# Performance work log

Measured on AMD Instinct MI355X. Metric: run time of the kernel, lower is better.

## Reference

```python
import jax, jax.numpy as jnp
import numpy as np

N_NODES = 50000
N_EDGES = 500000
D_FEAT = 128


def setup_inputs() -> dict:
    key = jax.random.key(0)
    k1, k2, k3 = jax.random.split(key, 3)
    r = jax.random.normal(k1, (N_NODES, D_FEAT), dtype=jnp.float32)
    e = jax.random.normal(k2, (N_EDGES, D_FEAT), dtype=jnp.float32)
    a = jax.random.randint(k3, (N_EDGES, 2), 0, N_NODES, dtype=jnp.int64)
    return {"r": r, "e": e, "a": a}


def reference(r, e, a):
    # message: gather source/target node features along edges, scale by edge feats
    rij = r[a[:, 0]] * e  # [E, D] messages src -> dst
    rji = r[a[:, 1]] * e  # [E, D] messages dst -> src
    # aggregate: scatter_add into node dimension (fixed num_segments for jit)
    out = jax.ops.segment_sum(rij, a[:, 1], num_segments=r.shape[0])
    out = out + jax.ops.segment_sum(rji, a[:, 0], num_segments=r.shape[0])
    return out  # [N, D]
```

## Files before the change

kernel.cpp:

```cpp
#include <hip/hip_runtime.h>


#define D_FEAT 128
#define SCAN_TILE 1024

__device__ inline unsigned bf16pack2(float a, float b) {
    unsigned ua = __float_as_uint(a), ub = __float_as_uint(b);
    ua += 0x7fffu + ((ua >> 16) & 1u);
    ub += 0x7fffu + ((ub >> 16) & 1u);
    return ((ua >> 16) & 0xffffu) | (ub & 0xffff0000u);
}

__global__ void prep_kernel(const float* __restrict__ e,
                            const float* __restrict__ r,
                            const int* __restrict__ a,
                            uint2* __restrict__ e16,
                            uint2* __restrict__ r16,
                            int* __restrict__ deg,
                            int n_e4, int n_r4, int n_entries) {
    int gid = blockIdx.x * blockDim.x + threadIdx.x;
    if (gid < n_entries) atomicAdd(&deg[a[gid]], 1);
    if (gid < n_r4) {
        const float4 v = ((const float4*)r)[gid];
        uint2 p;
        p.x = bf16pack2(v.x, v.y);
        p.y = bf16pack2(v.z, v.w);
        r16[gid] = p;
    }
    if (gid >= n_e4) return;
    const float4 v = ((const float4*)e)[gid];
    uint2 p;
    p.x = bf16pack2(v.x, v.y);
    p.y = bf16pack2(v.z, v.w);
    e16[gid] = p;
}

__global__ void scanA_kernel(const int* __restrict__ deg, int* __restrict__ bsum,
                             int n) {
    __shared__ int wsum[16];
    int t = threadIdx.x, lane = t & 63, w = t >> 6;
    int i = blockIdx.x * SCAN_TILE + t;
    int v = (i < n) ? deg[i] : 0;
    #pragma unroll
    for (int off = 32; off > 0; off >>= 1) v += __shfl_down(v, off, 64);
    if (lane == 0) wsum[w] = v;
    __syncthreads();
    if (t == 0) {
        int s = 0;
        #pragma unroll
        for (int k = 0; k < 16; ++k) s += wsum[k];
        bsum[blockIdx.x] = s;
    }
}

__global__ void scanB_kernel(int* __restrict__ bsum, int* __restrict__ bbase,
                             int* __restrict__ offs, int nblk, int n) {
    if (threadIdx.x == 0) {
        int run = 0;
        for (int b = 0; b < nblk; ++b) {
            bbase[b] = run;
            run += bsum[b];
        }
        offs[n] = run;
    }
}

__global__ void scanC_kernel(int* __restrict__ deg, int* __restrict__ offs,
                             const int* __restrict__ bbase, int n) {
    __shared__ int wsum[16];
    int t = threadIdx.x, lane = t & 63, w = t >> 6;
    int i = blockIdx.x * SCAN_TILE + t;
    int v = (i < n) ? deg[i] : 0;
    int x = v;
    #pragma unroll
    for (int off = 1; off < 64; off <<= 1) {
        int y = __shfl_up(x, off, 64);
        if (lane >= off) x += y;
    }
    if (lane == 63) wsum[w] = x;
    __syncthreads();
    if (w == 0 && lane < 16) {
        int s = wsum[lane];
        #pragma unroll
        for (int off = 1; off < 16; off <<= 1) {
            int y = __shfl_up(s, off, 64);
            if (lane >= off) s += y;
        }
        wsum[lane] = s;
    }
    __syncthreads();
    int wbase = (w == 0) ? 0 : wsum[w - 1];
    if (i < n) {
        int excl = x - v + wbase + bbase[blockIdx.x];
        offs[i] = excl;
        deg[i] = excl;
    }
}

__global__ void fill_kernel(const int* __restrict__ a, int* __restrict__ cursor,
                            int2* __restrict__ pl, int n_entries) {
    int k = blockIdx.x * blockDim.x + threadIdx.x;
    if (k >= n_entries) return;
    int edge = k >> 1, j = k & 1;
    int other  = a[2 * edge + j];
    int center = a[2 * edge + (j ^ 1)];
    int pos = atomicAdd(&cursor[center], 1);
    pl[pos] = make_int2(edge, other);
}

__global__ __launch_bounds__(256) void gather_kernel(
    const unsigned* __restrict__ e16, const unsigned* __restrict__ r16,
    const int* __restrict__ offs, const int2* __restrict__ pl,
    float* __restrict__ out, int n_nodes) {
    int n = blockIdx.x * 4 + (threadIdx.x >> 6);
    if (n >= n_nodes) return;
    int lane = threadIdx.x & 63;
    int start = offs[n];
    int end = offs[n + 1];
    float accx = 0.f, accy = 0.f;
    int i = start;
    for (; i + 4 <= end; i += 4) {
        int2 p0 = pl[i];
        int2 p1 = pl[i + 1];
        int2 p2 = pl[i + 2];
        int2 p3 = pl[i + 3];
        unsigned ew0 = e16[(size_t)p0.x * 64 + lane];
        unsigned rw0 = r16[(size_t)p0.y * 64 + lane];
        unsigned ew1 = e16[(size_t)p1.x * 64 + lane];
        unsigned rw1 = r16[(size_t)p1.y * 64 + lane];
        unsigned ew2 = e16[(size_t)p2.x * 64 + lane];
        unsigned rw2 = r16[(size_t)p2.y * 64 + lane];
        unsigned ew3 = e16[(size_t)p3.x * 64 + lane];
        unsigned rw3 = r16[(size_t)p3.y * 64 + lane];
        accx += __uint_as_float(ew0 << 16) * __uint_as_float(rw0 << 16);
        accy += __uint_as_float(ew0 & 0xffff0000u) * __uint_as_float(rw0 & 0xffff0000u);
        accx += __uint_as_float(ew1 << 16) * __uint_as_float(rw1 << 16);
        accy += __uint_as_float(ew1 & 0xffff0000u) * __uint_as_float(rw1 & 0xffff0000u);
        accx += __uint_as_float(ew2 << 16) * __uint_as_float(rw2 << 16);
        accy += __uint_as_float(ew2 & 0xffff0000u) * __uint_as_float(rw2 & 0xffff0000u);
        accx += __uint_as_float(ew3 << 16) * __uint_as_float(rw3 << 16);
        accy += __uint_as_float(ew3 & 0xffff0000u) * __uint_as_float(rw3 & 0xffff0000u);
    }
    for (; i < end; ++i) {
        int2 p0 = pl[i];
        unsigned ew0 = e16[(size_t)p0.x * 64 + lane];
        unsigned rw0 = r16[(size_t)p0.y * 64 + lane];
        accx += __uint_as_float(ew0 << 16) * __uint_as_float(rw0 << 16);
        accy += __uint_as_float(ew0 & 0xffff0000u) * __uint_as_float(rw0 & 0xffff0000u);
    }
    float2 res;
    res.x = accx;
    res.y = accy;
    *((float2*)(out + (size_t)n * D_FEAT) + lane) = res;
}

__global__ void hist_kernel(const int* __restrict__ a, int* __restrict__ deg,
                            int n_elems) {
    int i = blockIdx.x * blockDim.x + threadIdx.x;
    if (i < n_elems) atomicAdd(&deg[a[i]], 1);
}

__global__ __launch_bounds__(256) void gather_f32_kernel(
    const float* __restrict__ r, const float* __restrict__ e,
    const int* __restrict__ offs, const int2* __restrict__ pl,
    float* __restrict__ out, int n_nodes) {
    int n = blockIdx.x * 4 + (threadIdx.x >> 6);
    if (n >= n_nodes) return;
    int lane = threadIdx.x & 63;
    int start = offs[n];
    int end = offs[n + 1];
    float accx = 0.f, accy = 0.f;
    for (int i = start; i < end; ++i) {
        int2 p0 = pl[i];
        float2 ev0 = *((const float2*)(e + (size_t)p0.x * D_FEAT) + lane);
        float2 rv0 = *((const float2*)(r + (size_t)p0.y * D_FEAT) + lane);
        accx += ev0.x * rv0.x;
        accy += ev0.y * rv0.y;
    }
    float2 res;
    res.x = accx;
    res.y = accy;
    *((float2*)(out + (size_t)n * D_FEAT) + lane) = res;
}

__global__ void mp_scatter_kernel(const float* __restrict__ r,
                                  const float* __restrict__ e,
                                  const int* __restrict__ a,
                                  float* __restrict__ out,
                                  int n_edges) {
    long long gid = (long long)blockIdx.x * blockDim.x + threadIdx.x;
    int edge = (int)(gid >> 7);
    int feat = (int)(gid & 127);
    if (edge >= n_edges) return;
    int s = a[2 * edge];
    int d = a[2 * edge + 1];
    float ev = e[(long long)edge * D_FEAT + feat];
    float rs = r[(long long)s * D_FEAT + feat];
    float rd = r[(long long)d * D_FEAT + feat];
    atomicAdd(&out[(long long)d * D_FEAT + feat], rs * ev);
    atomicAdd(&out[(long long)s * D_FEAT + feat], rd * ev);
}

extern "C" void kernel_launch(void* const* d_in, const int* in_sizes, int n_in,
                              void* d_out, int out_size, void* d_ws, size_t ws_size,
                              hipStream_t stream) {
    const float* r = (const float*)d_in[0];
    const float* e = (const float*)d_in[1];
    const int*   a = (const int*)d_in[2];
    float* out = (float*)d_out;

    int n_nodes   = in_sizes[0] / D_FEAT;
    int n_edges   = in_sizes[1] / D_FEAT;
    int n_entries = 2 * n_edges;
    int n_e4      = in_sizes[1] / 4;
    int n_r4      = in_sizes[0] / 4;

    int block = 256;
    int grid_e = (n_entries + block - 1) / block;
    int nblk_scan = (n_nodes + SCAN_TILE - 1) / SCAN_TILE;

    {
        size_t ints_head = (size_t)n_nodes + (size_t)(n_nodes + 1)
                         + 2 * (size_t)nblk_scan;
        ints_head = (ints_head + 1) & ~(size_t)1;
        size_t need = ((size_t)n_e4 + (size_t)n_r4) * sizeof(uint2)
                    + ints_head * sizeof(int)
                    + (size_t)n_entries * sizeof(int2);
        if (ws_size >= need && nblk_scan <= 1024) {
            uint2* e16  = (uint2*)d_ws;
            uint2* r16  = e16 + n_e4;
            int*   deg  = (int*)(r16 + n_r4);
            int*   offs = deg + n_nodes;
            int*   bsum = offs + n_nodes + 1;
            int*   bbase= bsum + nblk_scan;
            int2*  pl   = (int2*)((int*)(r16 + n_r4) + ints_head);

            hipMemsetAsync(deg, 0, (size_t)n_nodes * sizeof(int), stream);
            int grid_p = (n_e4 + block - 1) / block;
            prep_kernel<<<grid_p, block, 0, stream>>>(e, r, a, e16, r16, deg,
                                                      n_e4, n_r4, n_entries);
            scanA_kernel<<<nblk_scan, SCAN_TILE, 0, stream>>>(deg, bsum, n_nodes);
            scanB_kernel<<<1, 64, 0, stream>>>(bsum, bbase, offs, nblk_scan,
                                               n_nodes);
            scanC_kernel<<<nblk_scan, SCAN_TILE, 0, stream>>>(deg, offs, bbase,
                                                              n_nodes);
            fill_kernel<<<grid_e, block, 0, stream>>>(a, deg, pl, n_entries);
            int grid_g = (n_nodes + 3) / 4;
            gather_kernel<<<grid_g, 256, 0, stream>>>(
                (const unsigned*)e16, (const unsigned*)r16, offs, pl, out,
                n_nodes);
            return;
        }
    }

    {
        size_t ints_head = (size_t)n_nodes + (size_t)(n_nodes + 1)
                         + 2 * (size_t)nblk_scan;
        ints_head = (ints_head + 1) & ~(size_t)1;
        size_t need = ints_head * sizeof(int) + (size_t)n_entries * sizeof(int2);
        if (ws_size >= need && nblk_scan <= 1024) {
            int*  deg  = (int*)d_ws;
            int*  offs = deg + n_nodes;
            int*  bsum = offs + n_nodes + 1;
            int*  bbase= bsum + nblk_scan;
            int2* pl   = (int2*)((int*)d_ws + ints_head);

            hipMemsetAsync(deg, 0, (size_t)n_nodes * sizeof(int), stream);
            hist_kernel<<<grid_e, block, 0, stream>>>(a, deg, n_entries);
            scanA_kernel<<<nblk_scan, SCAN_TILE, 0, stream>>>(deg, bsum, n_nodes);
            scanB_kernel<<<1, 64, 0, stream>>>(bsum, bbase, offs, nblk_scan,
                                               n_nodes);
            scanC_kernel<<<nblk_scan, SCAN_TILE, 0, stream>>>(deg, offs, bbase,
                                                              n_nodes);
            fill_kernel<<<grid_e, block, 0, stream>>>(a, deg, pl, n_entries);
            int grid_g = (n_nodes + 3) / 4;
            gather_f32_kernel<<<grid_g, 256, 0, stream>>>(r, e, offs, pl, out,
                                                          n_nodes);
            return;
        }
    }

    hipMemsetAsync(d_out, 0, (size_t)out_size * sizeof(float), stream);
    long long total = (long long)n_edges * D_FEAT;
    long long grid = (total + block - 1) / block;
    mp_scatter_kernel<<<(int)grid, block, 0, stream>>>(r, e, a, out, n_edges);
}
```

Before: 550.2 us.

## Materialize per-edge fp16 messages in CSR order, then sum contiguously per node

Adds a path where each edge computes both of its messages from the fp32 inputs. It packs them to fp16 and writes them into slots taken from the per-node cursor, so the messages land grouped by destination node. A second kernel then reduces each node's contiguous message rows. This swaps the random gather of bf16 edge rows for a large scatter write plus a sequential read. It needs a workspace of about 256 MB and changes the reduced-precision format from bf16 to fp16.

New measurement: 596.3 us. 1.08x slower.

```diff
diff --git a/kernel.cpp b/kernel.cpp
--- a/kernel.cpp
+++ b/kernel.cpp
@@ -1,8 +1,20 @@
 #include <hip/hip_runtime.h>
+#include <hip/hip_fp16.h>
 
 
 #define D_FEAT 128
 #define SCAN_TILE 1024
+
+__device__ inline unsigned pack_h2(float a, float b) {
+    __half2 h;
+    h.x = __float2half_rn(a);
+    h.y = __float2half_rn(b);
+    return *reinterpret_cast<unsigned*>(&h);
+}
+__device__ inline float2 unpack_h2(unsigned u) {
+    __half2 h = *reinterpret_cast<__half2*>(&u);
+    return __half22float2(h);
+}
 
 __device__ inline unsigned bf16pack2(float a, float b) {
     unsigned ua = __float_as_uint(a), ub = __float_as_uint(b);
@@ -10,6 +22,131 @@
     ub += 0x7fffu + ((ub >> 16) & 1u);
     return ((ua >> 16) & 0xffffu) | (ub & 0xffff0000u);
 }
+
+__global__ void hist_kernel(const int* __restrict__ a, int* __restrict__ deg,
+                            int n_elems) {
+    int i = blockIdx.x * blockDim.x + threadIdx.x;
+    if (i < n_elems) atomicAdd(&deg[a[i]], 1);
+}
+
+__global__ void scanA_kernel(const int* __restrict__ deg, int* __restrict__ bsum,
+                             int n) {
+    __shared__ int wsum[16];
+    int t = threadIdx.x, lane = t & 63, w = t >> 6;
+    int i = blockIdx.x * SCAN_TILE + t;
+    int v = (i < n) ? deg[i] : 0;
+    #pragma unroll
+    for (int off = 32; off > 0; off >>= 1) v += __shfl_down(v, off, 64);
+    if (lane == 0) wsum[w] = v;
+    __syncthreads();
+    if (t == 0) {
+        int s = 0;
+        #pragma unroll
+        for (int k = 0; k < 16; ++k) s += wsum[k];
+        bsum[blockIdx.x] = s;
+    }
+}
+
+__global__ void scanB_kernel(int* __restrict__ bsum, int* __restrict__ bbase,
+                             int* __restrict__ offs, int nblk, int n) {
+    if (threadIdx.x == 0) {
+        int run = 0;
+        for (int b = 0; b < nblk; ++b) {
+            bbase[b] = run;
+            run += bsum[b];
+        }
+        offs[n] = run;
+    }
+}
+
+__global__ void scanC_kernel(int* __restrict__ deg, int* __restrict__ offs,
+                             const int* __restrict__ bbase, int n) {
+    __shared__ int wsum[16];
+    int t = threadIdx.x, lane = t & 63, w = t >> 6;
+    int i = blockIdx.x * SCAN_TILE + t;
+    int v = (i < n) ? deg[i] : 0;
+    int x = v;
+    #pragma unroll
+    for (int off = 1; off < 64; off <<= 1) {
+        int y = __shfl_up(x, off, 64);
+        if (lane >= off) x += y;
+    }
+    if (lane == 63) wsum[w] = x;
+    __syncthreads();
+    if (w == 0 && lane < 16) {
+        int s = wsum[lane];
+        #pragma unroll
+        for (int off = 1; off < 16; off <<= 1) {
+            int y = __shfl_up(s, off, 64);
+            if (lane >= off) s += y;
+        }
+        wsum[lane] = s;
+    }
+    __syncthreads();
+    int wbase = (w == 0) ? 0 : wsum[w - 1];
+    if (i < n) {
+        int excl = x - v + wbase + bbase[blockIdx.x];
+        offs[i] = excl;
+        deg[i] = excl;
+    }
+}
+
+__global__ __launch_bounds__(256) void msg_kernel(
+    const float* __restrict__ r, const float* __restrict__ e,
+    const int* __restrict__ a, int* __restrict__ cursor,
+    unsigned* __restrict__ msg, int n_edges) {
+    int k = blockIdx.x * 4 + (threadIdx.x >> 6);
+    if (k >= n_edges) return;
+    int lane = threadIdx.x & 63;
+    int s = a[2 * k];
+    int d = a[2 * k + 1];
+    int p0 = 0, p1 = 0;
+    if (lane == 0) {
+        p0 = atomicAdd(&cursor[d], 1);
+        p1 = atomicAdd(&cursor[s], 1);
+    }
+    float2 ev = *((const float2*)(e + (size_t)k * D_FEAT) + lane);
+    float2 rs = *((const float2*)(r + (size_t)s * D_FEAT) + lane);
+    float2 rd = *((const float2*)(r + (size_t)d * D_FEAT) + lane);
+    p0 = __shfl(p0, 0, 64);
+    p1 = __shfl(p1, 0, 64);
+    msg[(size_t)p0 * 64 + lane] = pack_h2(ev.x * rs.x, ev.y * rs.y);
+    msg[(size_t)p1 * 64 + lane] = pack_h2(ev.x * rd.x, ev.y * rd.y);
+}
+
+__global__ __launch_bounds__(256) void sum_kernel(
+    const unsigned* __restrict__ msg, const int* __restrict__ offs,
+    float* __restrict__ out, int n_nodes) {
+    int n = blockIdx.x * 4 + (threadIdx.x >> 6);
+    if (n >= n_nodes) return;
+    int lane = threadIdx.x & 63;
+    int start = offs[n];
+    int end = offs[n + 1];
+    float accx = 0.f, accy = 0.f;
+    int i = start;
+    for (; i + 4 <= end; i += 4) {
+        unsigned u0 = msg[(size_t)(i + 0) * 64 + lane];
+        unsigned u1 = msg[(size_t)(i + 1) * 64 + lane];
+        unsigned u2 = msg[(size_t)(i + 2) * 64 + lane];
+        unsigned u3 = msg[(size_t)(i + 3) * 64 + lane];
+        float2 f0 = unpack_h2(u0);
+        float2 f1 = unpack_h2(u1);
+        float2 f2 = unpack_h2(u2);
+        float2 f3 = unpack_h2(u3);
+        accx += f0.x + f1.x + f2.x + f3.x;
+        accy += f0.y + f1.y + f2.y + f3.y;
+    }
+    for (; i < end; ++i) {
+        float2 f0 = unpack_h2(msg[(size_t)i * 64 + lane]);
+        accx += f0.x;
+        accy += f0.y;
+    }
+    float2 res;
+    res.x = accx;
+    res.y = accy;
+    *((float2*)(out + (size_t)n * D_FEAT) + lane) = res;
+}
+
 
 __global__ void prep_kernel(const float* __restrict__ e,
                             const float* __restrict__ r,
@@ -33,68 +170,6 @@
     p.x = bf16pack2(v.x, v.y);
     p.y = bf16pack2(v.z, v.w);
     e16[gid] = p;
-}
-
-__global__ void scanA_kernel(const int* __restrict__ deg, int* __restrict__ bsum,
-                             int n) {
-    __shared__ int wsum[16];
-    int t = threadIdx.x, lane = t & 63, w = t >> 6;
-    int i = blockIdx.x * SCAN_TILE + t;
-    int v = (i < n) ? deg[i] : 0;
-    #pragma unroll
-    for (int off = 32; off > 0; off >>= 1) v += __shfl_down(v, off, 64);
-    if (lane == 0) wsum[w] = v;
-    __syncthreads();
-    if (t == 0) {
-        int s = 0;
-        #pragma unroll
-        for (int k = 0; k < 16; ++k) s += wsum[k];
-        bsum[blockIdx.x] = s;
-    }
-}
-
-__global__ void scanB_kernel(int* __restrict__ bsum, int* __restrict__ bbase,
-                             int* __restrict__ offs, int nblk, int n) {
-    if (threadIdx.x == 0) {
-        int run = 0;
-        for (int b = 0; b < nblk; ++b) {
-            bbase[b] = run;
-            run += bsum[b];
-        }
-        offs[n] = run;
-    }
-}
-
-__global__ void scanC_kernel(int* __restrict__ deg, int* __restrict__ offs,
-                             const int* __restrict__ bbase, int n) {
-    __shared__ int wsum[16];
-    int t = threadIdx.x, lane = t & 63, w = t >> 6;
-    int i = blockIdx.x * SCAN_TILE + t;
-    int v = (i < n) ? deg[i] : 0;
-    int x = v;
-    #pragma unroll
-    for (int off = 1; off < 64; off <<= 1) {
-        int y = __shfl_up(x, off, 64);
-        if (lane >= off) x += y;
-    }
-    if (lane == 63) wsum[w] = x;
-    __syncthreads();
-    if (w == 0 && lane < 16) {
-        int s = wsum[lane];
-        #pragma unroll
-        for (int off = 1; off < 16; off <<= 1) {
-            int y = __shfl_up(s, off, 64);
-            if (lane >= off) s += y;
-        }
-        wsum[lane] = s;
-    }
-    __syncthreads();
-    int wbase = (w == 0) ? 0 : wsum[w - 1];
-    if (i < n) {
-        int excl = x - v + wbase + bbase[blockIdx.x];
-        offs[i] = excl;
-        deg[i] = excl;
-    }
 }
 
 __global__ void fill_kernel(const int* __restrict__ a, int* __restrict__ cursor,
@@ -154,12 +229,6 @@
     *((float2*)(out + (size_t)n * D_FEAT) + lane) = res;
 }
 
-__global__ void hist_kernel(const int* __restrict__ a, int* __restrict__ deg,
-                            int n_elems) {
-    int i = blockIdx.x * blockDim.x + threadIdx.x;
-    if (i < n_elems) atomicAdd(&deg[a[i]], 1);
-}
-
 __global__ __launch_bounds__(256) void gather_f32_kernel(
     const float* __restrict__ r, const float* __restrict__ e,
     const int* __restrict__ offs, const int2* __restrict__ pl,
@@ -222,6 +291,34 @@
     {
         size_t ints_head = (size_t)n_nodes + (size_t)(n_nodes + 1)
                          + 2 * (size_t)nblk_scan;
+        ints_head = (ints_head + 63) & ~(size_t)63;
+        size_t need = ints_head * sizeof(int)
+                    + (size_t)n_entries * 64 * sizeof(unsigned);
+        if (ws_size >= need && nblk_scan <= 1024) {
+            int* deg   = (int*)d_ws;
+            int* offs  = deg + n_nodes;
+            int* bsum  = offs + n_nodes + 1;
+            int* bbase = bsum + nblk_scan;
+            unsigned* msg = (unsigned*)((int*)d_ws + ints_head);
+
+            hipMemsetAsync(deg, 0, (size_t)n_nodes * sizeof(int), stream);
+            hist_kernel<<<grid_e, block, 0, stream>>>(a, deg, n_entries);
+            scanA_kernel<<<nblk_scan, SCAN_TILE, 0, stream>>>(deg, bsum, n_nodes);
+            scanB_kernel<<<1, 64, 0, stream>>>(bsum, bbase, offs, nblk_scan,
+                                               n_nodes);
+            scanC_kernel<<<nblk_scan, SCAN_TILE, 0, stream>>>(deg, offs, bbase,
+                                                              n_nodes);
+            int grid_m = (n_edges + 3) / 4;
+            msg_kernel<<<grid_m, 256, 0, stream>>>(r, e, a, deg, msg, n_edges);
+            int grid_g = (n_nodes + 3) / 4;
+            sum_kernel<<<grid_g, 256, 0, stream>>>(msg, offs, out, n_nodes);
+            return;
+        }
+    }
+
+    {
+        size_t ints_head = (size_t)n_nodes + (size_t)(n_nodes + 1)
+                         + 2 * (size_t)nblk_scan;
         ints_head = (ints_head + 1) & ~(size_t)1;
         size_t need = ((size_t)n_e4 + (size_t)n_r4) * sizeof(uint2)
                     + ints_head * sizeof(int)
```

## Pad degree counters to cache-line stride and switch staging precision to fp16

Applied to the files above, without the earlier changes.

Spreads each node's degree/cursor counter across a 32-int (128-byte) stride so atomics from the histogram and fill kernels land on separate cache lines, aiming to reduce atomic contention. It also replaces bf16 packing with fp16 conversion for the staged edge and node features, which improves mantissa precision but risks overflow or underflow for large or tiny values. The counter memset and scan reads grow by the stride factor, so the scans now make strided, uncoalesced loads.

After: 561.5 us. +2.1%, slower.

```diff
diff --git a/kernel.cpp b/kernel.cpp
--- a/kernel.cpp
+++ b/kernel.cpp
@@ -1,14 +1,20 @@
 #include <hip/hip_runtime.h>
+#include <hip/hip_fp16.h>
 
 
 #define D_FEAT 128
 #define SCAN_TILE 1024
-
-__device__ inline unsigned bf16pack2(float a, float b) {
-    unsigned ua = __float_as_uint(a), ub = __float_as_uint(b);
-    ua += 0x7fffu + ((ua >> 16) & 1u);
-    ub += 0x7fffu + ((ub >> 16) & 1u);
-    return ((ua >> 16) & 0xffffu) | (ub & 0xffff0000u);
+#define CSTRIDE 32
+
+__device__ inline unsigned pack_h2(float a, float b) {
+    __half2 h;
+    h.x = __float2half_rn(a);
+    h.y = __float2half_rn(b);
+    return *reinterpret_cast<unsigned*>(&h);
+}
+__device__ inline float2 unpack_h2(unsigned u) {
+    __half2 h = *reinterpret_cast<__half2*>(&u);
+    return __half22float2(h);
 }
 
 __global__ void prep_kernel(const float* __restrict__ e,
@@ -16,31 +22,37 @@
                             const int* __restrict__ a,
                             uint2* __restrict__ e16,
                             uint2* __restrict__ r16,
-                            int* __restrict__ deg,
-                            int n_e4, int n_r4, int n_entries) {
+                            int* __restrict__ degp,
+                            int n_e4, int n_r4, int n_entries, int cstride) {
     int gid = blockIdx.x * blockDim.x + threadIdx.x;
-    if (gid < n_entries) atomicAdd(&deg[a[gid]], 1);
+    if (gid < n_entries) atomicAdd(&degp[(size_t)a[gid] * cstride], 1);
     if (gid < n_r4) {
         const float4 v = ((const float4*)r)[gid];
         uint2 p;
-        p.x = bf16pack2(v.x, v.y);
-        p.y = bf16pack2(v.z, v.w);
+        p.x = pack_h2(v.x, v.y);
+        p.y = pack_h2(v.z, v.w);
         r16[gid] = p;
     }
     if (gid >= n_e4) return;
     const float4 v = ((const float4*)e)[gid];
     uint2 p;
-    p.x = bf16pack2(v.x, v.y);
-    p.y = bf16pack2(v.z, v.w);
+    p.x = pack_h2(v.x, v.y);
+    p.y = pack_h2(v.z, v.w);
     e16[gid] = p;
 }
 
-__global__ void scanA_kernel(const int* __restrict__ deg, int* __restrict__ bsum,
-                             int n) {
+__global__ void hist_kernel(const int* __restrict__ a, int* __restrict__ degp,
+                            int n_elems, int cstride) {
+    int i = blockIdx.x * blockDim.x + threadIdx.x;
+    if (i < n_elems) atomicAdd(&degp[(size_t)a[i] * cstride], 1);
+}
+
+__global__ void scanA_kernel(const int* __restrict__ degp, int* __restrict__ bsum,
+                             int n, int cstride) {
     __shared__ int wsum[16];
     int t = threadIdx.x, lane = t & 63, w = t >> 6;
     int i = blockIdx.x * SCAN_TILE + t;
-    int v = (i < n) ? deg[i] : 0;
+    int v = (i < n) ? degp[(size_t)i * cstride] : 0;
     #pragma unroll
     for (int off = 32; off > 0; off >>= 1) v += __shfl_down(v, off, 64);
     if (lane == 0) wsum[w] = v;
@@ -65,12 +77,12 @@
     }
 }
 
-__global__ void scanC_kernel(int* __restrict__ deg, int* __restrict__ offs,
-                             const int* __restrict__ bbase, int n) {
+__global__ void scanC_kernel(int* __restrict__ degp, int* __restrict__ offs,
+                             const int* __restrict__ bbase, int n, int cstride) {
     __shared__ int wsum[16];
     int t = threadIdx.x, lane = t & 63, w = t >> 6;
     int i = blockIdx.x * SCAN_TILE + t;
-    int v = (i < n) ? deg[i] : 0;
+    int v = (i < n) ? degp[(size_t)i * cstride] : 0;
     int x = v;
     #pragma unroll
     for (int off = 1; off < 64; off <<= 1) {
@@ -93,18 +105,18 @@
     if (i < n) {
         int excl = x - v + wbase + bbase[blockIdx.x];
         offs[i] = excl;
-        deg[i] = excl;
-    }
-}
-
-__global__ void fill_kernel(const int* __restrict__ a, int* __restrict__ cursor,
-                            int2* __restrict__ pl, int n_entries) {
+        degp[(size_t)i * cstride] = excl;
+    }
+}
+
+__global__ void fill_kernel(const int* __restrict__ a, int* __restrict__ cursorp,
+                            int2* __restrict__ pl, int n_entries, int cstride) {
     int k = blockIdx.x * blockDim.x + threadIdx.x;
     if (k >= n_entries) return;
     int edge = k >> 1, j = k & 1;
     int other  = a[2 * edge + j];
     int center = a[2 * edge + (j ^ 1)];
-    int pos = atomicAdd(&cursor[center], 1);
+    int pos = atomicAdd(&cursorp[(size_t)center * cstride], 1);
     pl[pos] = make_int2(edge, other);
 }
 
@@ -132,32 +144,26 @@
         unsigned rw2 = r16[(size_t)p2.y * 64 + lane];
         unsigned ew3 = e16[(size_t)p3.x * 64 + lane];
         unsigned rw3 = r16[(size_t)p3.y * 64 + lane];
-        accx += __uint_as_float(ew0 << 16) * __uint_as_float(rw0 << 16);
-        accy += __uint_as_float(ew0 & 0xffff0000u) * __uint_as_float(rw0 & 0xffff0000u);
-        accx += __uint_as_float(ew1 << 16) * __uint_as_float(rw1 << 16);
-        accy += __uint_as_float(ew1 & 0xffff0000u) * __uint_as_float(rw1 & 0xffff0000u);
-        accx += __uint_as_float(ew2 << 16) * __uint_as_float(rw2 << 16);
-        accy += __uint_as_float(ew2 & 0xffff0000u) * __uint_as_float(rw2 & 0xffff0000u);
-        accx += __uint_as_float(ew3 << 16) * __uint_as_float(rw3 << 16);
-        accy += __uint_as_float(ew3 & 0xffff0000u) * __uint_as_float(rw3 & 0xffff0000u);
+        float2 e0 = unpack_h2(ew0), r0 = unpack_h2(rw0);
+        float2 e1 = unpack_h2(ew1), r1 = unpack_h2(rw1);
+        float2 e2 = unpack_h2(ew2), r2 = unpack_h2(rw2);
+        float2 e3 = unpack_h2(ew3), r3 = unpack_h2(rw3);
+        accx += e0.x * r0.x; accy += e0.y * r0.y;
+        accx += e1.x * r1.x; accy += e1.y * r1.y;
+        accx += e2.x * r2.x; accy += e2.y * r2.y;
+        accx += e3.x * r3.x; accy += e3.y * r3.y;
     }
     for (; i < end; ++i) {
         int2 p0 = pl[i];
         unsigned ew0 = e16[(size_t)p0.x * 64 + lane];
         unsigned rw0 = r16[(size_t)p0.y * 64 + lane];
-        accx += __uint_as_float(ew0 << 16) * __uint_as_float(rw0 << 16);
-        accy += __uint_as_float(ew0 & 0xffff0000u) * __uint_as_float(rw0 & 0xffff0000u);
+        float2 e0 = unpack_h2(ew0), r0 = unpack_h2(rw0);
+        accx += e0.x * r0.x; accy += e0.y * r0.y;
     }
     float2 res;
     res.x = accx;
     res.y = accy;
     *((float2*)(out + (size_t)n * D_FEAT) + lane) = res;
-}
-
-__global__ void hist_kernel(const int* __restrict__ a, int* __restrict__ deg,
-                            int n_elems) {
-    int i = blockIdx.x * blockDim.x + threadIdx.x;
-    if (i < n_elems) atomicAdd(&deg[a[i]], 1);
 }
 
 __global__ __launch_bounds__(256) void gather_f32_kernel(
@@ -220,7 +226,7 @@
     int nblk_scan = (n_nodes + SCAN_TILE - 1) / SCAN_TILE;
 
     {
-        size_t ints_head = (size_t)n_nodes + (size_t)(n_nodes + 1)
+        size_t ints_head = (size_t)CSTRIDE * n_nodes + (size_t)(n_nodes + 1)
                          + 2 * (size_t)nblk_scan;
         ints_head = (ints_head + 1) & ~(size_t)1;
         size_t need = ((size_t)n_e4 + (size_t)n_r4) * sizeof(uint2)
@@ -229,22 +235,26 @@
         if (ws_size >= need && nblk_scan <= 1024) {
             uint2* e16  = (uint2*)d_ws;
             uint2* r16  = e16 + n_e4;
-            int*   deg  = (int*)(r16 + n_r4);
-            int*   offs = deg + n_nodes;
+            int*   degp = (int*)(r16 + n_r4);
+            int*   offs = degp + (size_t)CSTRIDE * n_nodes;
             int*   bsum = offs + n_nodes + 1;
             int*   bbase= bsum + nblk_scan;
             int2*  pl   = (int2*)((int*)(r16 + n_r4) + ints_head);
 
-            hipMemsetAsync(deg, 0, (size_t)n_nodes * sizeof(int), stream);
+            hipMemsetAsync(degp, 0, (size_t)CSTRIDE * n_nodes * sizeof(int),
+                           stream);
             int grid_p = (n_e4 + block - 1) / block;
-            prep_kernel<<<grid_p, block, 0, stream>>>(e, r, a, e16, r16, deg,
-                                                      n_e4, n_r4, n_entries);
-            scanA_kernel<<<nblk_scan, SCAN_TILE, 0, stream>>>(deg, bsum, n_nodes);
+            prep_kernel<<<grid_p, block, 0, stream>>>(e, r, a, e16, r16, degp,
+                                                      n_e4, n_r4, n_entries,
+                                                      CSTRIDE);
+            scanA_kernel<<<nblk_scan, SCAN_TILE, 0, stream>>>(degp, bsum,
+                                                              n_nodes, CSTRIDE);
             scanB_kernel<<<1, 64, 0, stream>>>(bsum, bbase, offs, nblk_scan,
                                                n_nodes);
-            scanC_kernel<<<nblk_scan, SCAN_TILE, 0, stream>>>(deg, offs, bbase,
-                                                              n_nodes);
-            fill_kernel<<<grid_e, block, 0, stream>>>(a, deg, pl, n_entries);
+            scanC_kernel<<<nblk_scan, SCAN_TILE, 0, stream>>>(degp, offs, bbase,
+                                                              n_nodes, CSTRIDE);
+            fill_kernel<<<grid_e, block, 0, stream>>>(a, degp, pl, n_entries,
+                                                      CSTRIDE);
             int grid_g = (n_nodes + 3) / 4;
             gather_kernel<<<grid_g, 256, 0, stream>>>(
                 (const unsigned*)e16, (const unsigned*)r16, offs, pl, out,
@@ -254,29 +264,37 @@
     }
 
     {
-        size_t ints_head = (size_t)n_nodes + (size_t)(n_nodes + 1)
-                         + 2 * (size_t)nblk_scan;
-        ints_head = (ints_head + 1) & ~(size_t)1;
-        size_t need = ints_head * sizeof(int) + (size_t)n_entries * sizeof(int2);
-        if (ws_size >= need && nblk_scan <= 1024) {
-            int*  deg  = (int*)d_ws;
-            int*  offs = deg + n_nodes;
-            int*  bsum = offs + n_nodes + 1;
-            int*  bbase= bsum + nblk_scan;
-            int2* pl   = (int2*)((int*)d_ws + ints_head);
-
-            hipMemsetAsync(deg, 0, (size_t)n_nodes * sizeof(int), stream);
-            hist_kernel<<<grid_e, block, 0, stream>>>(a, deg, n_entries);
-            scanA_kernel<<<nblk_scan, SCAN_TILE, 0, stream>>>(deg, bsum, n_nodes);
-            scanB_kernel<<<1, 64, 0, stream>>>(bsum, bbase, offs, nblk_scan,
-                                               n_nodes);
-            scanC_kernel<<<nblk_scan, SCAN_TILE, 0, stream>>>(deg, offs, bbase,
-                                                              n_nodes);
-            fill_kernel<<<grid_e, block, 0, stream>>>(a, deg, pl, n_entries);
-            int grid_g = (n_nodes + 3) / 4;
-            gather_f32_kernel<<<grid_g, 256, 0, stream>>>(r, e, offs, pl, out,
-                                                          n_nodes);
-            return;
+        for (int cs = CSTRIDE; cs >= 1; cs = (cs == CSTRIDE) ? 1 : 0) {
+            size_t ints_head = (size_t)cs * n_nodes + (size_t)(n_nodes + 1)
+                             + 2 * (size_t)nblk_scan;
+            ints_head = (ints_head + 1) & ~(size_t)1;
+            size_t need = ints_head * sizeof(int)
+                        + (size_t)n_entries * sizeof(int2);
+            if (ws_size >= need && nblk_scan <= 1024) {
+                int*  degp = (int*)d_ws;
+                int*  offs = degp + (size_t)cs * n_nodes;
+                int*  bsum = offs + n_nodes + 1;
+                int*  bbase= bsum + nblk_scan;
+                int2* pl   = (int2*)((int*)d_ws + ints_head);
+
+                hipMemsetAsync(degp, 0, (size_t)cs * n_nodes * sizeof(int),
+                               stream);
+                hist_kernel<<<grid_e, block, 0, stream>>>(a, degp, n_entries, cs);
+                scanA_kernel<<<nblk_scan, SCAN_TILE, 0, stream>>>(degp, bsum,
+                                                                  n_nodes, cs);
+                scanB_kernel<<<1, 64, 0, stream>>>(bsum, bbase, offs, nblk_scan,
+                                                   n_nodes);
+                scanC_kernel<<<nblk_scan, SCAN_TILE, 0, stream>>>(degp, offs,
+                                                                  bbase, n_nodes,
+                                                                  cs);
+                fill_kernel<<<grid_e, block, 0, stream>>>(a, degp, pl, n_entries,
+                                                          cs);
+                int grid_g = (n_nodes + 3) / 4;
+                gather_f32_kernel<<<grid_g, 256, 0, stream>>>(r, e, offs, pl,
+                                                              out, n_nodes);
+                return;
+            }
+            if (cs == 1) break;
         }
     }
 
```

## Replace global-atomic CSR build with per-chunk LDS histograms and deterministic fill

Applied to the files above, without the earlier changes.

Builds the CSR adjacency by giving each 4096-entry chunk its own shared-memory histogram of packed 8-bit counters. A merge kernel turns these into per-chunk base offsets, and the fill kernel then places entries using shared-memory atomics, so no global atomics remain. Edge and node features are also converted to fp16 instead of bf16. The goal is to avoid global atomic contention in the hist and fill stages. In exchange it adds a large per-chunk base array (about 245 chunks × 50000 ints) that merge writes and fill reads, and it relies on 8-bit counters not overflowing.

New measurement: 549.8 us. Within noise of the previous version (-0.1%).

```diff
diff --git a/kernel.cpp b/kernel.cpp
--- a/kernel.cpp
+++ b/kernel.cpp
@@ -1,38 +1,73 @@
 #include <hip/hip_runtime.h>
+#include <hip/hip_fp16.h>
 
 
 #define D_FEAT 128
 #define SCAN_TILE 1024
-
-__device__ inline unsigned bf16pack2(float a, float b) {
-    unsigned ua = __float_as_uint(a), ub = __float_as_uint(b);
-    ua += 0x7fffu + ((ua >> 16) & 1u);
-    ub += 0x7fffu + ((ub >> 16) & 1u);
-    return ((ua >> 16) & 0xffffu) | (ub & 0xffff0000u);
+#define CHUNK 4096
+
+__device__ inline unsigned pack_h2(float a, float b) {
+    __half2 h;
+    h.x = __float2half_rn(a);
+    h.y = __float2half_rn(b);
+    return *reinterpret_cast<unsigned*>(&h);
+}
+__device__ inline float2 unpack_h2(unsigned u) {
+    __half2 h = *reinterpret_cast<__half2*>(&u);
+    return __half22float2(h);
 }
 
 __global__ void prep_kernel(const float* __restrict__ e,
                             const float* __restrict__ r,
-                            const int* __restrict__ a,
                             uint2* __restrict__ e16,
                             uint2* __restrict__ r16,
-                            int* __restrict__ deg,
-                            int n_e4, int n_r4, int n_entries) {
+                            int n_e4, int n_r4) {
     int gid = blockIdx.x * blockDim.x + threadIdx.x;
-    if (gid < n_entries) atomicAdd(&deg[a[gid]], 1);
     if (gid < n_r4) {
         const float4 v = ((const float4*)r)[gid];
         uint2 p;
-        p.x = bf16pack2(v.x, v.y);
-        p.y = bf16pack2(v.z, v.w);
+        p.x = pack_h2(v.x, v.y);
+        p.y = pack_h2(v.z, v.w);
         r16[gid] = p;
     }
     if (gid >= n_e4) return;
     const float4 v = ((const float4*)e)[gid];
     uint2 p;
-    p.x = bf16pack2(v.x, v.y);
-    p.y = bf16pack2(v.z, v.w);
+    p.x = pack_h2(v.x, v.y);
+    p.y = pack_h2(v.z, v.w);
     e16[gid] = p;
+}
+
+__global__ __launch_bounds__(256) void hist1_kernel(
+    const int* __restrict__ a, unsigned* __restrict__ ghist,
+    int n_entries, int nwords) {
+    extern __shared__ unsigned h[];
+    for (int i = threadIdx.x; i < nwords; i += blockDim.x) h[i] = 0u;
+    __syncthreads();
+    int s = blockIdx.x * CHUNK;
+    int e = s + CHUNK;
+    if (e > n_entries) e = n_entries;
+    for (int idx = s + threadIdx.x; idx < e; idx += blockDim.x) {
+        int n = a[idx];
+        atomicAdd(&h[n >> 2], 1u << ((n & 3) * 8));
+    }
+    __syncthreads();
+    unsigned* dst = ghist + (size_t)blockIdx.x * nwords;
+    for (int i = threadIdx.x; i < nwords; i += blockDim.x) dst[i] = h[i];
+}
+
+__global__ void merge2_kernel(const unsigned* __restrict__ ghist,
+                              int* __restrict__ base, int* __restrict__ deg,
+                              int n_nodes, int nblk, int nwords) {
+    int n = blockIdx.x * blockDim.x + threadIdx.x;
+    if (n >= n_nodes) return;
+    int w = n >> 2, sh = (n & 3) * 8;
+    int run = 0;
+    for (int b = 0; b < nblk; ++b) {
+        base[(size_t)b * n_nodes + n] = run;
+        run += (int)((ghist[(size_t)b * nwords + w] >> sh) & 0xffu);
+    }
+    deg[n] = run;
 }
 
 __global__ void scanA_kernel(const int* __restrict__ deg, int* __restrict__ bsum,
@@ -65,7 +100,7 @@
     }
 }
 
-__global__ void scanC_kernel(int* __restrict__ deg, int* __restrict__ offs,
+__global__ void scanC_kernel(const int* __restrict__ deg, int* __restrict__ offs,
                              const int* __restrict__ bbase, int n) {
     __shared__ int wsum[16];
     int t = threadIdx.x, lane = t & 63, w = t >> 6;
@@ -90,22 +125,29 @@
     }
     __syncthreads();
     int wbase = (w == 0) ? 0 : wsum[w - 1];
-    if (i < n) {
-        int excl = x - v + wbase + bbase[blockIdx.x];
-        offs[i] = excl;
-        deg[i] = excl;
-    }
-}
-
-__global__ void fill_kernel(const int* __restrict__ a, int* __restrict__ cursor,
-                            int2* __restrict__ pl, int n_entries) {
-    int k = blockIdx.x * blockDim.x + threadIdx.x;
-    if (k >= n_entries) return;
-    int edge = k >> 1, j = k & 1;
-    int other  = a[2 * edge + j];
-    int center = a[2 * edge + (j ^ 1)];
-    int pos = atomicAdd(&cursor[center], 1);
-    pl[pos] = make_int2(edge, other);
+    if (i < n) offs[i] = x - v + wbase + bbase[blockIdx.x];
+}
+
+__global__ __launch_bounds__(256) void fill3_kernel(
+    const int* __restrict__ a, const int* __restrict__ offs,
+    const int* __restrict__ base, int2* __restrict__ pl,
+    int n_entries, int n_nodes, int nwords) {
+    extern __shared__ unsigned cur[];
+    for (int i = threadIdx.x; i < nwords; i += blockDim.x) cur[i] = 0u;
+    __syncthreads();
+    int s = blockIdx.x * CHUNK;
+    int e = s + CHUNK;
+    if (e > n_entries) e = n_entries;
+    const int* brow = base + (size_t)blockIdx.x * n_nodes;
+    for (int idx = s + threadIdx.x; idx < e; idx += blockDim.x) {
+        int other  = a[idx];
+        int center = a[idx ^ 1];
+        int sh = (center & 3) * 8;
+        unsigned old = atomicAdd(&cur[center >> 2], 1u << sh);
+        int local = (int)((old >> sh) & 0xffu);
+        int pos = offs[center] + brow[center] + local;
+        pl[pos] = make_int2(idx >> 1, other);
+    }
 }
 
 __global__ __launch_bounds__(256) void gather_kernel(
@@ -132,21 +174,21 @@
         unsigned rw2 = r16[(size_t)p2.y * 64 + lane];
         unsigned ew3 = e16[(size_t)p3.x * 64 + lane];
         unsigned rw3 = r16[(size_t)p3.y * 64 + lane];
-        accx += __uint_as_float(ew0 << 16) * __uint_as_float(rw0 << 16);
-        accy += __uint_as_float(ew0 & 0xffff0000u) * __uint_as_float(rw0 & 0xffff0000u);
-        accx += __uint_as_float(ew1 << 16) * __uint_as_float(rw1 << 16);
-        accy += __uint_as_float(ew1 & 0xffff0000u) * __uint_as_float(rw1 & 0xffff0000u);
-        accx += __uint_as_float(ew2 << 16) * __uint_as_float(rw2 << 16);
-        accy += __uint_as_float(ew2 & 0xffff0000u) * __uint_as_float(rw2 & 0xffff0000u);
-        accx += __uint_as_float(ew3 << 16) * __uint_as_float(rw3 << 16);
-        accy += __uint_as_float(ew3 & 0xffff0000u) * __uint_as_float(rw3 & 0xffff0000u);
+        float2 e0 = unpack_h2(ew0), r0 = unpack_h2(rw0);
+        float2 e1 = unpack_h2(ew1), r1 = unpack_h2(rw1);
+        float2 e2 = unpack_h2(ew2), r2 = unpack_h2(rw2);
+        float2 e3 = unpack_h2(ew3), r3 = unpack_h2(rw3);
+        accx += e0.x * r0.x; accy += e0.y * r0.y;
+        accx += e1.x * r1.x; accy += e1.y * r1.y;
+        accx += e2.x * r2.x; accy += e2.y * r2.y;
+        accx += e3.x * r3.x; accy += e3.y * r3.y;
     }
     for (; i < end; ++i) {
         int2 p0 = pl[i];
         unsigned ew0 = e16[(size_t)p0.x * 64 + lane];
         unsigned rw0 = r16[(size_t)p0.y * 64 + lane];
-        accx += __uint_as_float(ew0 << 16) * __uint_as_float(rw0 << 16);
-        accy += __uint_as_float(ew0 & 0xffff0000u) * __uint_as_float(rw0 & 0xffff0000u);
+        float2 e0 = unpack_h2(ew0), r0 = unpack_h2(rw0);
+        accx += e0.x * r0.x; accy += e0.y * r0.y;
     }
     float2 res;
     res.x = accx;
@@ -154,10 +196,54 @@
     *((float2*)(out + (size_t)n * D_FEAT) + lane) = res;
 }
 
+
 __global__ void hist_kernel(const int* __restrict__ a, int* __restrict__ deg,
                             int n_elems) {
     int i = blockIdx.x * blockDim.x + threadIdx.x;
     if (i < n_elems) atomicAdd(&deg[a[i]], 1);
+}
+
+__global__ void fill_kernel(const int* __restrict__ a, int* __restrict__ cursor,
+                            int2* __restrict__ pl, int n_entries) {
+    int k = blockIdx.x * blockDim.x + threadIdx.x;
+    if (k >= n_entries) return;
+    int edge = k >> 1, j = k & 1;
+    int other  = a[2 * edge + j];
+    int center = a[2 * edge + (j ^ 1)];
+    int pos = atomicAdd(&cursor[center], 1);
+    pl[pos] = make_int2(edge, other);
+}
+
+__global__ void scanC_cursor_kernel(int* __restrict__ deg, int* __restrict__ offs,
+                                    const int* __restrict__ bbase, int n) {
+    __shared__ int wsum[16];
+    int t = threadIdx.x, lane = t & 63, w = t >> 6;
+    int i = blockIdx.x * SCAN_TILE + t;
+    int v = (i < n) ? deg[i] : 0;
+    int x = v;
+    #pragma unroll
+    for (int off = 1; off < 64; off <<= 1) {
+        int y = __shfl_up(x, off, 64);
+        if (lane >= off) x += y;
+    }
+    if (lane == 63) wsum[w] = x;
+    __syncthreads();
+    if (w == 0 && lane < 16) {
+        int s = wsum[lane];
+        #pragma unroll
+        for (int off = 1; off < 16; off <<= 1) {
+            int y = __shfl_up(s, off, 64);
+            if (lane >= off) s += y;
+        }
+        wsum[lane] = s;
+    }
+    __syncthreads();
+    int wbase = (w == 0) ? 0 : wsum[w - 1];
+    if (i < n) {
+        int excl = x - v + wbase + bbase[blockIdx.x];
+        offs[i] = excl;
+        deg[i] = excl;
+    }
 }
 
 __global__ __launch_bounds__(256) void gather_f32_kernel(
@@ -218,33 +304,49 @@
     int block = 256;
     int grid_e = (n_entries + block - 1) / block;
     int nblk_scan = (n_nodes + SCAN_TILE - 1) / SCAN_TILE;
+    int nblk_c = (n_entries + CHUNK - 1) / CHUNK;
+    int nwords = (n_nodes + 3) / 4;
+    size_t lds_bytes = (size_t)nwords * sizeof(unsigned);
 
     {
-        size_t ints_head = (size_t)n_nodes + (size_t)(n_nodes + 1)
+        size_t ints_head = (size_t)nblk_c * nwords + (size_t)nblk_c * n_nodes
+                         + (size_t)n_nodes + (size_t)(n_nodes + 1)
                          + 2 * (size_t)nblk_scan;
         ints_head = (ints_head + 1) & ~(size_t)1;
         size_t need = ((size_t)n_e4 + (size_t)n_r4) * sizeof(uint2)
                     + ints_head * sizeof(int)
                     + (size_t)n_entries * sizeof(int2);
-        if (ws_size >= need && nblk_scan <= 1024) {
-            uint2* e16  = (uint2*)d_ws;
-            uint2* r16  = e16 + n_e4;
-            int*   deg  = (int*)(r16 + n_r4);
-            int*   offs = deg + n_nodes;
-            int*   bsum = offs + n_nodes + 1;
-            int*   bbase= bsum + nblk_scan;
-            int2*  pl   = (int2*)((int*)(r16 + n_r4) + ints_head);
-
-            hipMemsetAsync(deg, 0, (size_t)n_nodes * sizeof(int), stream);
-            int grid_p = (n_e4 + block - 1) / block;
-            prep_kernel<<<grid_p, block, 0, stream>>>(e, r, a, e16, r16, deg,
-                                                      n_e4, n_r4, n_entries);
-            scanA_kernel<<<nblk_scan, SCAN_TILE, 0, stream>>>(deg, bsum, n_nodes);
+        if (ws_size >= need && nblk_scan <= 1024 && lds_bytes <= 64 * 1024) {
+            uint2* e16   = (uint2*)d_ws;
+            uint2* r16   = e16 + n_e4;
+            unsigned* ghist = (unsigned*)(r16 + n_r4);
+            int*   basep = (int*)(ghist + (size_t)nblk_c * nwords);
+            int*   deg   = basep + (size_t)nblk_c * n_nodes;
+            int*   offs  = deg + n_nodes;
+            int*   bsum  = offs + n_nodes + 1;
+            int*   bbase = bsum + nblk_scan;
+            int2*  pl    = (int2*)((int*)(r16 + n_r4) + ints_head);
+
+            int grid_p = (n_e4 > n_r4 ? n_e4 : n_r4);
+            grid_p = (grid_p + block - 1) / block;
+            prep_kernel<<<grid_p, block, 0, stream>>>(e, r, e16, r16,
+                                                      n_e4, n_r4);
+            hist1_kernel<<<nblk_c, block, lds_bytes, stream>>>(a, ghist,
+                                                               n_entries,
+                                                               nwords);
+            int grid_m = (n_nodes + block - 1) / block;
+            merge2_kernel<<<grid_m, block, 0, stream>>>(ghist, basep, deg,
+                                                        n_nodes, nblk_c,
+                                                        nwords);
+            scanA_kernel<<<nblk_scan, SCAN_TILE, 0, stream>>>(deg, bsum,
+                                                              n_nodes);
             scanB_kernel<<<1, 64, 0, stream>>>(bsum, bbase, offs, nblk_scan,
                                                n_nodes);
             scanC_kernel<<<nblk_scan, SCAN_TILE, 0, stream>>>(deg, offs, bbase,
                                                               n_nodes);
-            fill_kernel<<<grid_e, block, 0, stream>>>(a, deg, pl, n_entries);
+            fill3_kernel<<<nblk_c, block, lds_bytes, stream>>>(a, offs, basep,
+                                                               pl, n_entries,
+                                                               n_nodes, nwords);
             int grid_g = (n_nodes + 3) / 4;
             gather_kernel<<<grid_g, 256, 0, stream>>>(
                 (const unsigned*)e16, (const unsigned*)r16, offs, pl, out,
@@ -270,8 +372,9 @@
             scanA_kernel<<<nblk_scan, SCAN_TILE, 0, stream>>>(deg, bsum, n_nodes);
             scanB_kernel<<<1, 64, 0, stream>>>(bsum, bbase, offs, nblk_scan,
                                                n_nodes);
-            scanC_kernel<<<nblk_scan, SCAN_TILE, 0, stream>>>(deg, offs, bbase,
-                                                              n_nodes);
+            scanC_cursor_kernel<<<nblk_scan, SCAN_TILE, 0, stream>>>(deg, offs,
+                                                                     bbase,
+                                                                     n_nodes);
             fill_kernel<<<grid_e, block, 0, stream>>>(a, deg, pl, n_entries);
             int grid_g = (n_nodes + 3) / 4;
             gather_f32_kernel<<<grid_g, 256, 0, stream>>>(r, e, offs, pl, out,
```
